# Optimization experiments

Measured on AMD Instinct MI355X. Metric: run time of the kernel, lower is better.

## Reference

```python
import jax, jax.numpy as jnp
import numpy as np

CODEBOOK_SIZE = 1024
EMBEDDING_DIM = 64


def setup_inputs() -> dict:
    key = jax.random.key(0)
    k_in, k_cb = jax.random.split(key)
    # latent feature (batch, embedding_dim, length)
    input = jax.random.normal(k_in, (16, EMBEDDING_DIM, 8192), dtype=jnp.float32)
    # learned codebook table (codebook_size, embedding_dim)
    codebook = jax.random.normal(k_cb, (CODEBOOK_SIZE, EMBEDDING_DIM), dtype=jnp.float32)
    return {"input": input, "codebook": codebook}


def reference(input, codebook):
    # input: (B, D, T); codebook: (K, D)
    B, D = input.shape[0], input.shape[1]
    spatial = input.shape[2:]
    # move embedding dim last and flatten tokens: (B*T, D)
    x = jnp.moveaxis(input, 1, -1).reshape(-1, D)
    x_sq = jnp.sum(x * x, axis=-1, keepdims=True)            # (N, 1)
    e_sq = jnp.sum(codebook * codebook, axis=-1)             # (K,)
    dist = x_sq - 2.0 * (x @ codebook.T) + e_sq[None, :]     # (N, K)
    indices = jnp.argmin(dist, axis=-1)                      # (N,)
    quantized = jnp.take(codebook, indices, axis=0)          # (N, D)
    # reshape back: output (B, D, *spatial), indices (B, *spatial)
    out = jnp.moveaxis(quantized.reshape((B,) + spatial + (D,)), -1, 1)
    idx = indices.reshape((B,) + spatial)
    return out, idx
```

## Files before the change

kernel.cpp:

```cpp
#include <hip/hip_runtime.h>
#include <float.h>

#define K_CODES 1024
#define DIM 64
#define T_LEN 8192
#define N_TOK 131072
#define LO_SCALE 2048.0f

typedef _Float16 half8 __attribute__((ext_vector_type(8)));
typedef float    f32x4 __attribute__((ext_vector_type(4)));

#define MFMA16(a, b, c) __builtin_amdgcn_mfma_f32_16x16x32_f16((a), (b), (c), 0, 0, 0)

__global__ void vq_prep(const float* __restrict__ cb,
                        _Float16* __restrict__ w,
                        float* __restrict__ wesq) {
    __shared__ float part[128];
    const int ct   = blockIdx.x;
    const int r    = threadIdx.x;
    const int halF = r >> 7;
    const int rr   = r & 127;
    const int q    = rr >> 4;
    const int code = rr & 15;

    const float* src = cb + (size_t)(ct * 16 + code) * DIM + q * 8;
    float4 v0 = *reinterpret_cast<const float4*>(src);
    float4 v1 = *reinterpret_cast<const float4*>(src + 4);
    float x[8] = {v0.x, v0.y, v0.z, v0.w, v1.x, v1.y, v1.z, v1.w};

    half8 o;
    float psum = 0.0f;
    #pragma unroll
    for (int j = 0; j < 8; ++j) {
        _Float16 h = (_Float16)x[j];
        o[j] = halF ? (_Float16)((x[j] - (float)h) * LO_SCALE) : h;
        psum = fmaf(x[j], x[j], psum);
    }
    *reinterpret_cast<half8*>(w + (size_t)ct * 2048 + halF * 1024 + q * 128 + code * 8) = o;

    if (halF == 0) part[rr] = psum;
    __syncthreads();
    if (r < 16) {
        float s = 0.0f;
        #pragma unroll
        for (int q2 = 0; q2 < 8; ++q2) s += part[q2 * 16 + r];
        wesq[ct * 16 + r] = s * LO_SCALE;
    }
}

__global__ __launch_bounds__(256, 2)
void vq_main(const float* __restrict__ in,
             const float* __restrict__ cb,
             const _Float16* __restrict__ w,
             const float* __restrict__ wesq,
             float* __restrict__ out) {
    __shared__ float esq_s[K_CODES];
    __shared__ int   idx_s[256];

    const int tid  = threadIdx.x;
    const int wave = tid >> 6;
    const int lane = tid & 63;
    const int lo4  = lane & 15;
    const int quad = lane >> 4;

    for (int k = tid; k < K_CODES; k += 256) esq_s[k] = wesq[k];
    __syncthreads();

    const int strip = blockIdx.x * 256 + wave * 64;
    const int b  = strip >> 13;
    const int t0 = strip & 8191;

    const float* xin = in + (size_t)b * DIM * T_LEN + t0;
    half8 a_h[4][2], a_hs[4][2], a_l[4][2];
    #pragma unroll
    for (int mt = 0; mt < 4; ++mt) {
        #pragma unroll
        for (int s = 0; s < 2; ++s) {
            half8 hh, hs, ll;
            #pragma unroll
            for (int j = 0; j < 8; ++j) {
                const int d = s * 32 + quad * 8 + j;
                float xv = -2.0f * xin[(size_t)d * T_LEN + mt * 16 + lo4];
                _Float16 h = (_Float16)xv;
                hh[j] = h;
                hs[j] = (_Float16)((float)h * LO_SCALE);
                ll[j] = (_Float16)((xv - (float)h) * LO_SCALE);
            }
            a_h[mt][s] = hh;
            a_hs[mt][s] = hs;
            a_l[mt][s] = ll;
        }
    }

    float best[16];
    int   bidx[16];
    #pragma unroll
    for (int i = 0; i < 16; ++i) { best[i] = FLT_MAX; bidx[i] = 0; }

    const _Float16* wb = w + (size_t)lane * 8;

    half8 Ah0, Ah1, Al0, Al1, Bh0, Bh1, Bl0, Bl1;
    float Ae, Be;
    auto loadB = [&](int ct, half8& h0, half8& h1, half8& l0, half8& l1, float& es) {
        const _Float16* p = wb + (size_t)ct * 2048;
        h0 = *reinterpret_cast<const half8*>(p);
        h1 = *reinterpret_cast<const half8*>(p + 512);
        l0 = *reinterpret_cast<const half8*>(p + 1024);
        l1 = *reinterpret_cast<const half8*>(p + 1536);
        es = esq_s[ct * 16 + lo4];
    };
    auto step = [&](const half8& h0, const half8& h1, const half8& l0,
                    const half8& l1, float es, int ct) {
        const int code = ct * 16 + lo4;
        #pragma unroll
        for (int mt = 0; mt < 4; ++mt) {
            f32x4 c = {es, es, es, es};
            c = MFMA16(a_hs[mt][0], h0, c);
            c = MFMA16(a_hs[mt][1], h1, c);
            c = MFMA16(a_h[mt][0], l0, c);
            c = MFMA16(a_h[mt][1], l1, c);
            c = MFMA16(a_l[mt][0], h0, c);
            c = MFMA16(a_l[mt][1], h1, c);
            #pragma unroll
            for (int r = 0; r < 4; ++r) {
                float sc = c[r];
                const int i = mt * 4 + r;
                bool lt = sc < best[i];
                best[i] = lt ? sc : best[i];
                bidx[i] = lt ? code : bidx[i];
            }
        }
    };

    loadB(0, Ah0, Ah1, Al0, Al1, Ae);
    loadB(1, Bh0, Bh1, Bl0, Bl1, Be);
    for (int p = 0; p < 31; ++p) {
        step(Ah0, Ah1, Al0, Al1, Ae, 2 * p);
        loadB(2 * p + 2, Ah0, Ah1, Al0, Al1, Ae);
        step(Bh0, Bh1, Bl0, Bl1, Be, 2 * p + 1);
        loadB(2 * p + 3, Bh0, Bh1, Bl0, Bl1, Be);
    }
    step(Ah0, Ah1, Al0, Al1, Ae, 62);
    step(Bh0, Bh1, Bl0, Bl1, Be, 63);

    #pragma unroll
    for (int i = 0; i < 16; ++i) {
        float s = best[i];
        int  ix = bidx[i];
        #pragma unroll
        for (int off = 1; off < 16; off <<= 1) {
            float s2 = __shfl_xor(s, off, 64);
            int  ix2 = __shfl_xor(ix, off, 64);
            bool take = (s2 < s) || (s2 == s && ix2 < ix);
            s  = take ? s2 : s;
            ix = take ? ix2 : ix;
        }
        if (lo4 == 0) {
            idx_s[wave * 64 + (i >> 2) * 16 + quad * 4 + (i & 3)] = ix;
        }
    }
    __syncthreads();

    const int token = blockIdx.x * 256 + tid;
    const int tb = token >> 13;
    const int tt = token & 8191;
    const int my_idx = idx_s[tid];

    out[(size_t)N_TOK * DIM + token] = (float)my_idx;

    const float* crow = cb + (size_t)my_idx * DIM;
    float* outv = out + (size_t)tb * DIM * T_LEN + tt;
    #pragma unroll
    for (int d0 = 0; d0 < DIM; d0 += 4) {
        float4 v = *reinterpret_cast<const float4*>(crow + d0);
        outv[(size_t)(d0 + 0) * T_LEN] = v.x;
        outv[(size_t)(d0 + 1) * T_LEN] = v.y;
        outv[(size_t)(d0 + 2) * T_LEN] = v.z;
        outv[(size_t)(d0 + 3) * T_LEN] = v.w;
    }
}

extern "C" void kernel_launch(void* const* d_in, const int* in_sizes, int n_in,
                              void* d_out, int out_size, void* d_ws, size_t ws_size,
                              hipStream_t stream) {
    const float* in = (const float*)d_in[0];
    const float* cb = (const float*)d_in[1];
    float* out = (float*)d_out;

    _Float16* w   = (_Float16*)d_ws;
    float*   wesq = (float*)((char*)d_ws + 64 * 4096);

    vq_prep<<<dim3(64), dim3(256), 0, stream>>>(cb, w, wesq);
    vq_main<<<dim3(N_TOK / 256), dim3(256), 0, stream>>>(in, cb, w, wesq, out);
}
```

Measured before the change: 129.0 us.

## Switch distance GEMM to 32x32x16 MFMA with 32-token strips per wave

Replaces the 16x16x32 MFMA tiling with 32x32x16 MFMAs, so each wave processes 32 tokens against 32-code tiles. The codebook prep layout is rebuilt to match, and B fragments are prefetched before the activation conversion. Staggered s_sleep per wave and s_setprio around the MFMA chain try to desynchronise waves and favour matrix issue. Blocks now cover 128 tokens, which doubles the grid, and the output gather is split across two halves of the block. The cost is more codebook-fragment loads per token and a longer shuffle reduction over 32 lanes.

```diff
diff --git a/kernel.cpp b/kernel.cpp
--- a/kernel.cpp
+++ b/kernel.cpp
@@ -7,44 +7,45 @@
 #define N_TOK 131072
 #define LO_SCALE 2048.0f
 
-typedef _Float16 half8 __attribute__((ext_vector_type(8)));
-typedef float    f32x4 __attribute__((ext_vector_type(4)));
-
-#define MFMA16(a, b, c) __builtin_amdgcn_mfma_f32_16x16x32_f16((a), (b), (c), 0, 0, 0)
+typedef _Float16 half8  __attribute__((ext_vector_type(8)));
+typedef float    f32x16 __attribute__((ext_vector_type(16)));
+
+#define MFMA32(a, b, c) __builtin_amdgcn_mfma_f32_32x32x16_f16((a), (b), (c), 0, 0, 0)
 
 __global__ void vq_prep(const float* __restrict__ cb,
                         _Float16* __restrict__ w,
                         float* __restrict__ wesq) {
-    __shared__ float part[128];
-    const int ct   = blockIdx.x;
-    const int r    = threadIdx.x;
-    const int halF = r >> 7;
-    const int rr   = r & 127;
-    const int q    = rr >> 4;
-    const int code = rr & 15;
-
-    const float* src = cb + (size_t)(ct * 16 + code) * DIM + q * 8;
+    __shared__ float part[256];
+    const int ct = blockIdx.x;
+    const int t  = threadIdx.x;
+    const int c  = t & 31;
+    const int kq = t >> 5;
+
+    const float* src = cb + (size_t)(ct * 32 + c) * DIM + kq * 8;
     float4 v0 = *reinterpret_cast<const float4*>(src);
     float4 v1 = *reinterpret_cast<const float4*>(src + 4);
     float x[8] = {v0.x, v0.y, v0.z, v0.w, v1.x, v1.y, v1.z, v1.w};
 
-    half8 o;
+    half8 oh, ol;
     float psum = 0.0f;
     #pragma unroll
     for (int j = 0; j < 8; ++j) {
         _Float16 h = (_Float16)x[j];
-        o[j] = halF ? (_Float16)((x[j] - (float)h) * LO_SCALE) : h;
+        oh[j] = h;
+        ol[j] = (_Float16)((x[j] - (float)h) * LO_SCALE);
         psum = fmaf(x[j], x[j], psum);
     }
-    *reinterpret_cast<half8*>(w + (size_t)ct * 2048 + halF * 1024 + q * 128 + code * 8) = o;
-
-    if (halF == 0) part[rr] = psum;
+    const size_t off = (size_t)ct * 4096 + (size_t)((kq >> 1) * 512 + (kq & 1) * 256 + c * 8);
+    *reinterpret_cast<half8*>(w + off)        = oh;
+    *reinterpret_cast<half8*>(w + off + 2048) = ol;
+
+    part[t] = psum;
     __syncthreads();
-    if (r < 16) {
+    if (t < 32) {
         float s = 0.0f;
         #pragma unroll
-        for (int q2 = 0; q2 < 8; ++q2) s += part[q2 * 16 + r];
-        wesq[ct * 16 + r] = s * LO_SCALE;
+        for (int kq2 = 0; kq2 < 8; ++kq2) s += part[kq2 * 32 + t];
+        wesq[ct * 32 + t] = s * LO_SCALE;
     }
 }
 
@@ -55,41 +56,62 @@
              const float* __restrict__ wesq,
              float* __restrict__ out) {
     __shared__ float esq_s[K_CODES];
-    __shared__ int   idx_s[256];
+    __shared__ int   idx_s[128];
 
     const int tid  = threadIdx.x;
     const int wave = tid >> 6;
     const int lane = tid & 63;
-    const int lo4  = lane & 15;
-    const int quad = lane >> 4;
+    const int col  = lane & 31;
+    const int o    = lane >> 5;
 
     for (int k = tid; k < K_CODES; k += 256) esq_s[k] = wesq[k];
     __syncthreads();
 
-    const int strip = blockIdx.x * 256 + wave * 64;
+    {
+        const int ph = ((blockIdx.x & 1) << 1) | (wave & 1);
+        if (ph == 1)      __builtin_amdgcn_s_sleep(4);
+        else if (ph == 2) __builtin_amdgcn_s_sleep(8);
+        else if (ph == 3) __builtin_amdgcn_s_sleep(12);
+    }
+
+    const int strip = blockIdx.x * 128 + wave * 32;
     const int b  = strip >> 13;
     const int t0 = strip & 8191;
 
+    const _Float16* wb = w + (size_t)lane * 8;
+
+    half8 Fh0[4], Fl0[4], Fh1[4], Fl1[4];
+    float e0, e1;
+    auto loadB = [&](int ct, half8 (&Fh)[4], half8 (&Fl)[4], float& es) {
+        const _Float16* p = wb + (size_t)ct * 4096;
+        #pragma unroll
+        for (int kf = 0; kf < 4; ++kf) {
+            Fh[kf] = *reinterpret_cast<const half8*>(p + kf * 512);
+            Fl[kf] = *reinterpret_cast<const half8*>(p + kf * 512 + 2048);
+        }
+        es = esq_s[ct * 32 + col];
+    };
+
+    loadB(0, Fh0, Fl0, e0);
+    loadB(1, Fh1, Fl1, e1);
+
     const float* xin = in + (size_t)b * DIM * T_LEN + t0;
-    half8 a_h[4][2], a_hs[4][2], a_l[4][2];
-    #pragma unroll
-    for (int mt = 0; mt < 4; ++mt) {
-        #pragma unroll
-        for (int s = 0; s < 2; ++s) {
-            half8 hh, hs, ll;
-            #pragma unroll
-            for (int j = 0; j < 8; ++j) {
-                const int d = s * 32 + quad * 8 + j;
-                float xv = -2.0f * xin[(size_t)d * T_LEN + mt * 16 + lo4];
-                _Float16 h = (_Float16)xv;
-                hh[j] = h;
-                hs[j] = (_Float16)((float)h * LO_SCALE);
-                ll[j] = (_Float16)((xv - (float)h) * LO_SCALE);
-            }
-            a_h[mt][s] = hh;
-            a_hs[mt][s] = hs;
-            a_l[mt][s] = ll;
-        }
+    half8 a_hs[4], a_h[4], a_l[4];
+    #pragma unroll
+    for (int kf = 0; kf < 4; ++kf) {
+        half8 hh, hs, ll;
+        #pragma unroll
+        for (int j = 0; j < 8; ++j) {
+            const int d = kf * 16 + o * 8 + j;
+            float xv = -2.0f * xin[(size_t)d * T_LEN + col];
+            _Float16 h = (_Float16)xv;
+            hh[j] = h;
+            hs[j] = (_Float16)((float)h * LO_SCALE);
+            ll[j] = (_Float16)((xv - (float)h) * LO_SCALE);
+        }
+        a_h[kf] = hh;
+        a_hs[kf] = hs;
+        a_l[kf] = ll;
     }
 
     float best[16];
@@ -97,81 +119,75 @@
     #pragma unroll
     for (int i = 0; i < 16; ++i) { best[i] = FLT_MAX; bidx[i] = 0; }
 
-    const _Float16* wb = w + (size_t)lane * 8;
-
-    half8 Ah0, Ah1, Al0, Al1, Bh0, Bh1, Bl0, Bl1;
-    float Ae, Be;
-    auto loadB = [&](int ct, half8& h0, half8& h1, half8& l0, half8& l1, float& es) {
-        const _Float16* p = wb + (size_t)ct * 2048;
-        h0 = *reinterpret_cast<const half8*>(p);
-        h1 = *reinterpret_cast<const half8*>(p + 512);
-        l0 = *reinterpret_cast<const half8*>(p + 1024);
-        l1 = *reinterpret_cast<const half8*>(p + 1536);
-        es = esq_s[ct * 16 + lo4];
+    auto step = [&](const half8 (&Fh)[4], const half8 (&Fl)[4], float es, int ct) {
+        const int code = ct * 32 + col;
+        f32x16 c;
+        #pragma unroll
+        for (int i = 0; i < 16; ++i) c[i] = es;
+        __builtin_amdgcn_s_setprio(1);
+        c = MFMA32(a_hs[0], Fh[0], c);
+        c = MFMA32(a_hs[1], Fh[1], c);
+        c = MFMA32(a_hs[2], Fh[2], c);
+        c = MFMA32(a_hs[3], Fh[3], c);
+        c = MFMA32(a_h[0], Fl[0], c);
+        c = MFMA32(a_h[1], Fl[1], c);
+        c = MFMA32(a_h[2], Fl[2], c);
+        c = MFMA32(a_h[3], Fl[3], c);
+        c = MFMA32(a_l[0], Fh[0], c);
+        c = MFMA32(a_l[1], Fh[1], c);
+        c = MFMA32(a_l[2], Fh[2], c);
+        c = MFMA32(a_l[3], Fh[3], c);
+        __builtin_amdgcn_s_setprio(0);
+        #pragma unroll
+        for (int r = 0; r < 16; ++r) {
+            float sc = c[r];
+            bool lt = sc < best[r];
+            best[r] = lt ? sc : best[r];
+            bidx[r] = lt ? code : bidx[r];
+        }
     };
-    auto step = [&](const half8& h0, const half8& h1, const half8& l0,
-                    const half8& l1, float es, int ct) {
-        const int code = ct * 16 + lo4;
-        #pragma unroll
-        for (int mt = 0; mt < 4; ++mt) {
-            f32x4 c = {es, es, es, es};
-            c = MFMA16(a_hs[mt][0], h0, c);
-            c = MFMA16(a_hs[mt][1], h1, c);
-            c = MFMA16(a_h[mt][0], l0, c);
-            c = MFMA16(a_h[mt][1], l1, c);
-            c = MFMA16(a_l[mt][0], h0, c);
-            c = MFMA16(a_l[mt][1], h1, c);
-            #pragma unroll
-            for (int r = 0; r < 4; ++r) {
-                float sc = c[r];
-                const int i = mt * 4 + r;
-                bool lt = sc < best[i];
-                best[i] = lt ? sc : best[i];
-                bidx[i] = lt ? code : bidx[i];
-            }
-        }
-    };
-
-    loadB(0, Ah0, Ah1, Al0, Al1, Ae);
-    loadB(1, Bh0, Bh1, Bl0, Bl1, Be);
-    for (int p = 0; p < 31; ++p) {
-        step(Ah0, Ah1, Al0, Al1, Ae, 2 * p);
-        loadB(2 * p + 2, Ah0, Ah1, Al0, Al1, Ae);
-        step(Bh0, Bh1, Bl0, Bl1, Be, 2 * p + 1);
-        loadB(2 * p + 3, Bh0, Bh1, Bl0, Bl1, Be);
-    }
-    step(Ah0, Ah1, Al0, Al1, Ae, 62);
-    step(Bh0, Bh1, Bl0, Bl1, Be, 63);
+
+    for (int p = 0; p < 15; ++p) {
+        step(Fh0, Fl0, e0, 2 * p);
+        loadB(2 * p + 2, Fh0, Fl0, e0);
+        step(Fh1, Fl1, e1, 2 * p + 1);
+        loadB(2 * p + 3, Fh1, Fl1, e1);
+    }
+    step(Fh0, Fl0, e0, 30);
+    step(Fh1, Fl1, e1, 31);
 
     #pragma unroll
     for (int i = 0; i < 16; ++i) {
         float s = best[i];
         int  ix = bidx[i];
         #pragma unroll
-        for (int off = 1; off < 16; off <<= 1) {
+        for (int off = 1; off < 32; off <<= 1) {
             float s2 = __shfl_xor(s, off, 64);
             int  ix2 = __shfl_xor(ix, off, 64);
             bool take = (s2 < s) || (s2 == s && ix2 < ix);
             s  = take ? s2 : s;
             ix = take ? ix2 : ix;
         }
-        if (lo4 == 0) {
-            idx_s[wave * 64 + (i >> 2) * 16 + quad * 4 + (i & 3)] = ix;
+        if (col == 0) {
+            idx_s[wave * 32 + (i & 3) + 8 * (i >> 2) + 4 * o] = ix;
         }
     }
     __syncthreads();
 
-    const int token = blockIdx.x * 256 + tid;
+    const int tok_l = tid & 127;
+    const int half_ = tid >> 7;
+    const int token = blockIdx.x * 128 + tok_l;
     const int tb = token >> 13;
     const int tt = token & 8191;
-    const int my_idx = idx_s[tid];
-
-    out[(size_t)N_TOK * DIM + token] = (float)my_idx;
-
-    const float* crow = cb + (size_t)my_idx * DIM;
-    float* outv = out + (size_t)tb * DIM * T_LEN + tt;
-    #pragma unroll
-    for (int d0 = 0; d0 < DIM; d0 += 4) {
+    const int my_idx = idx_s[tok_l];
+
+    if (half_ == 0)
+        out[(size_t)N_TOK * DIM + token] = (float)my_idx;
+
+    const float* crow = cb + (size_t)my_idx * DIM + half_ * 32;
+    float* outv = out + (size_t)tb * DIM * T_LEN + (size_t)(half_ * 32) * T_LEN + tt;
+    #pragma unroll
+    for (int d0 = 0; d0 < 32; d0 += 4) {
         float4 v = *reinterpret_cast<const float4*>(crow + d0);
         outv[(size_t)(d0 + 0) * T_LEN] = v.x;
         outv[(size_t)(d0 + 1) * T_LEN] = v.y;
@@ -190,6 +206,6 @@
     _Float16* w   = (_Float16*)d_ws;
     float*   wesq = (float*)((char*)d_ws + 64 * 4096);
 
-    vq_prep<<<dim3(64), dim3(256), 0, stream>>>(cb, w, wesq);
-    vq_main<<<dim3(N_TOK / 256), dim3(256), 0, stream>>>(in, cb, w, wesq, out);
+    vq_prep<<<dim3(32), dim3(256), 0, stream>>>(cb, w, wesq);
+    vq_main<<<dim3(N_TOK / 128), dim3(256), 0, stream>>>(in, cb, w, wesq, out);
 }
```

Result: slower. 149.0 us (+15.5%).
